# Performance work log

Hardware: AMD Instinct MI355X
Metric: run time of the kernel (lower is better)

Reference implementation:

```python
import jax, jax.numpy as jnp
import numpy as np

B, L, D, H = 2, 4096, 512, 8
DK = D // H
SCALE = 1.0 / float(np.sqrt(DK))


def setup_inputs() -> dict:
    key = jax.random.key(0)
    k1, k2, k3 = jax.random.split(key, 3)
    x = jax.random.normal(k1, (B, L, D), dtype=jnp.float32)
    w_qkv = jax.random.normal(k2, (3 * D, D), dtype=jnp.float32) * 0.02
    w_o = jax.random.normal(k3, (D, D), dtype=jnp.float32) * 0.02
    return {"x": x, "w_qkv": w_qkv, "w_o": w_o}


def reference(x, w_qkv, w_o):
    b, l, d = x.shape
    # qkv projection: Linear(d, 3d, bias=False) -> x @ W^T
    qkv = (x @ w_qkv.T).reshape(b, l, 3, H, DK).transpose(2, 0, 3, 1, 4)  # [3,B,H,L,dk]
    q, k, v = qkv[0], qkv[1], qkv[2]
    # naive O(L^2) attention (faithful to source)
    scores = jnp.einsum("bhld,bhmd->bhlm", q, k) * SCALE  # [B,H,L,L]
    attn = jax.nn.softmax(scores, axis=-1)
    ctx = jnp.einsum("bhlm,bhmd->bhld", attn, v)  # [B,H,L,dk]
    ctx = ctx.transpose(0, 2, 1, 3).reshape(b, l, d)
    return ctx @ w_o.T
```

## Files before the change

### kernel.cpp

```cpp
#include <hip/hip_runtime.h>


#define Bq 2
#define Lq 4096
#define Dq 512
#define Hq 8
#define DKq 64
#define PST 72

using short8  = __attribute__((ext_vector_type(8))) short;
using ushort8 = __attribute__((ext_vector_type(8))) unsigned short;
using float4v = __attribute__((ext_vector_type(4))) float;
using half4   = __attribute__((ext_vector_type(4))) _Float16;
typedef unsigned short u16;
typedef unsigned int   u32;

__device__ __forceinline__ u16 f2bf(float f) {
    u32 u = __float_as_uint(f);
    u += 0x7fffu + ((u >> 16) & 1u);
    return (u16)(u >> 16);
}

__device__ __forceinline__ float exp2fast(float x) {
#if __has_builtin(__builtin_amdgcn_exp2f)
    return __builtin_amdgcn_exp2f(x);
#else
    return exp2f(x);
#endif
}

__device__ __forceinline__ float4v mfma16(short8 a, short8 b, float4v c) {
    return __builtin_amdgcn_mfma_f32_16x16x32_bf16(a, b, c, 0, 0, 0);
}

__device__ __forceinline__ void gload_lds16(const u16* g, u16* l) {
    __builtin_amdgcn_global_load_lds(
        (const __attribute__((address_space(1))) unsigned int*)g,
        (__attribute__((address_space(3))) unsigned int*)l,
        16, 0, 0);
}

__global__ __launch_bounds__(256) void castall(const float* __restrict__ x,
                                               const float* __restrict__ wq,
                                               const float* __restrict__ wo,
                                               u16* __restrict__ xb,
                                               u16* __restrict__ wqb,
                                               u16* __restrict__ wob) {
    int g = blockIdx.x;
    const float* s; u16* d; int base;
    if (g < 4096)      { s = x;  d = xb;  base = g * 1024; }
    else if (g < 4864) { s = wq; d = wqb; base = (g - 4096) * 1024; }
    else               { s = wo; d = wob; base = (g - 4864) * 1024; }
    int i = base + threadIdx.x * 4;
    float4 f = *(const float4*)&s[i];
    ushort4 o;
    o.x = f2bf(f.x); o.y = f2bf(f.y); o.z = f2bf(f.z); o.w = f2bf(f.w);
    *(ushort4*)&d[i] = o;
}

__global__ __launch_bounds__(256) void qkv_gemm(const u16* __restrict__ A,
                                                const u16* __restrict__ Bw,
                                                u16* __restrict__ qb,
                                                u16* __restrict__ kb,
                                                u16* __restrict__ vt) {
    __shared__ __align__(16) union {
        struct { u16 A[128 * 64]; u16 B[128 * 64]; } s;
        u16 epi[128 * 134];
    } sm;
    const int m0 = blockIdx.x * 128, n0 = blockIdx.y * 128;
    const int tid = threadIdx.x, w = tid >> 6, lane = tid & 63;
    const int l15 = lane & 15, quad = lane >> 4;
    const int wy = w & 1, wx = w >> 1;
    const int r8 = lane >> 3, c8 = lane & 7, csw = c8 ^ r8;
    const int sw = l15 & 7;

    float4v acc[4][4];
    float4v zero = {0.f, 0.f, 0.f, 0.f};
#pragma unroll
    for (int mi = 0; mi < 4; mi++)
#pragma unroll
        for (int ni = 0; ni < 4; ni++) acc[mi][ni] = zero;

    for (int k0 = 0; k0 < 512; k0 += 64) {
#pragma unroll
        for (int i = 0; i < 4; i++) {
            int row = w * 32 + i * 8;
            gload_lds16(&A[(size_t)(m0 + row + r8) * 512 + k0 + csw * 8], &sm.s.A[row * 64]);
            gload_lds16(&Bw[(size_t)(n0 + row + r8) * 512 + k0 + csw * 8], &sm.s.B[row * 64]);
        }
        __syncthreads();
        short8 af0[4], af1[4], bf0[4], bf1[4];
#pragma unroll
        for (int t = 0; t < 4; t++) {
            int rowA = wy * 64 + t * 16 + l15;
            af0[t] = *(const short8*)&sm.s.A[rowA * 64 + ((quad ^ sw) * 8)];
            af1[t] = *(const short8*)&sm.s.A[rowA * 64 + (((quad + 4) ^ sw) * 8)];
            int rowB = wx * 64 + t * 16 + l15;
            bf0[t] = *(const short8*)&sm.s.B[rowB * 64 + ((quad ^ sw) * 8)];
            bf1[t] = *(const short8*)&sm.s.B[rowB * 64 + (((quad + 4) ^ sw) * 8)];
        }
#pragma unroll
        for (int mi = 0; mi < 4; mi++)
#pragma unroll
            for (int ni = 0; ni < 4; ni++) {
                acc[mi][ni] = mfma16(af0[mi], bf0[ni], acc[mi][ni]);
                acc[mi][ni] = mfma16(af1[mi], bf1[ni], acc[mi][ni]);
            }
        __syncthreads();
    }

    const int sel = n0 >> 9;
    if (sel < 2) {
        const float sc = (sel == 0) ? 0.18033688f : 1.0f;
#pragma unroll
        for (int mi = 0; mi < 4; mi++)
#pragma unroll
            for (int ni = 0; ni < 4; ni++)
#pragma unroll
                for (int r = 0; r < 4; r++)
                    sm.epi[(wy * 64 + mi * 16 + quad * 4 + r) * 134 + wx * 64 + ni * 16 + l15] =
                        f2bf(acc[mi][ni][r] * sc);
        __syncthreads();
        u16* tgt = (sel == 0) ? qb : kb;
#pragma unroll
        for (int i = 0; i < 8; i++) {
            int flat = i * 2048 + tid * 8;
            int row = flat >> 7, col = flat & 127;
            ushort8 vv = *(const ushort8*)&sm.epi[row * 134 + col];
            int dg = (n0 & 511) + col, h = dg >> 6, dk = dg & 63;
            int mm = m0 + row, b = mm >> 12, l = mm & 4095;
            *(ushort8*)&tgt[((size_t)(b * Hq + h) * Lq + l) * DKq + dk] = vv;
        }
    } else {
#pragma unroll
        for (int mi = 0; mi < 4; mi++)
#pragma unroll
            for (int ni = 0; ni < 4; ni++) {
                ushort4 v4;
                v4.x = f2bf(acc[mi][ni][0]); v4.y = f2bf(acc[mi][ni][1]);
                v4.z = f2bf(acc[mi][ni][2]); v4.w = f2bf(acc[mi][ni][3]);
                *(ushort4*)&sm.epi[(wx * 64 + ni * 16 + l15) * 134 + wy * 64 + mi * 16 + quad * 4] = v4;
            }
        __syncthreads();
#pragma unroll
        for (int i = 0; i < 8; i++) {
            int flat = i * 2048 + tid * 8;
            int vrow = flat >> 7, vcol = flat & 127;
            ushort8 vv = *(const ushort8*)&sm.epi[vrow * 134 + vcol];
            int dg = (n0 & 511) + vrow, h = dg >> 6, dk = dg & 63;
            int mm = m0 + vcol, b = mm >> 12, l = mm & 4095;
            *(ushort8*)&vt[((size_t)(b * Hq + h) * DKq + dk) * Lq + l] = vv;
        }
    }
}

__global__ __launch_bounds__(256, 4) void attn_kern(const u16* __restrict__ qb,
                                                    const u16* __restrict__ kb,
                                                    const u16* __restrict__ vt,
                                                    _Float16* __restrict__ op0,
                                                    _Float16* __restrict__ op1,
                                                    float* __restrict__ denp) {
    __shared__ __align__(16) u16 Ks[64 * 64];
    __shared__ __align__(16) u16 Vs[64 * 64];
    __shared__ __align__(16) u16 Ps[4 * 32 * PST];
    const int g = blockIdx.x;
    const int xcd = g & 7, idx = g >> 3;
    const int bh = xcd * 2 + (idx & 1);
    const int rest = idx >> 1;
    const int split = rest & 1;
    const int q0 = (rest >> 1) * 128;
    const int tid = threadIdx.x;
    const int w = tid >> 6, lane = tid & 63, l15 = lane & 15, quad = lane >> 4;
    const int r8 = lane >> 3, c8 = lane & 7, csw = c8 ^ r8;
    const int sw = l15 & 7;

    const u16* qbase = qb + (size_t)bh * Lq * DKq;
    const u16* kbase = kb + (size_t)bh * Lq * DKq;
    const u16* vbase = vt + (size_t)bh * DKq * Lq;

    short8 aq0[2], aq1[2];
#pragma unroll
    for (int s = 0; s < 2; s++) {
        int qrow = q0 + w * 32 + s * 16 + l15;
        aq0[s] = *(const short8*)&qbase[(size_t)qrow * DKq + quad * 8];
        aq1[s] = *(const short8*)&qbase[(size_t)qrow * DKq + 32 + quad * 8];
    }

    short8 ones8;
#pragma unroll
    for (int j = 0; j < 8; j++) ones8[j] = (short)0x3F80;

    float4v zero = {0.f, 0.f, 0.f, 0.f};
    float4v oacc[2][4], den[2];
#pragma unroll
    for (int s = 0; s < 2; s++) {
        den[s] = zero;
#pragma unroll
        for (int n = 0; n < 4; n++) oacc[s][n] = zero;
    }

    u16* Pw = Ps + w * 32 * PST;
    const int j0base = split * 2048;

    for (int jt = 0; jt < 32; jt++) {
        int j0 = j0base + jt * 64;
        if (w < 2) {
#pragma unroll
            for (int i = 0; i < 4; i++) {
                int base = w * 32 + i * 8;
                gload_lds16(&kbase[(size_t)(j0 + base + r8) * DKq + csw * 8], &Ks[base * 64]);
            }
        } else {
#pragma unroll
            for (int i = 0; i < 4; i++) {
                int base = (w - 2) * 32 + i * 8;
                gload_lds16(&vbase[(size_t)(base + r8) * Lq + j0 + csw * 8], &Vs[base * 64]);
            }
        }
        __syncthreads();

        short8 kf0[4], kf1[4], vf0[4], vf1[4];
#pragma unroll
        for (int n = 0; n < 4; n++) {
            int row = n * 16 + l15;
            kf0[n] = *(const short8*)&Ks[row * 64 + ((quad ^ sw) * 8)];
            kf1[n] = *(const short8*)&Ks[row * 64 + (((quad + 4) ^ sw) * 8)];
            vf0[n] = *(const short8*)&Vs[row * 64 + ((quad ^ sw) * 8)];
            vf1[n] = *(const short8*)&Vs[row * 64 + (((quad + 4) ^ sw) * 8)];
        }

#pragma unroll
        for (int s = 0; s < 2; s++) {
#pragma unroll
            for (int nk = 0; nk < 4; nk++) {
                float4v sv = zero;
                sv = mfma16(kf0[nk], aq0[s], sv);
                sv = mfma16(kf1[nk], aq1[s], sv);
                u32 u0 = __float_as_uint(exp2fast(sv[0])) + 0x8000u;
                u32 u1 = __float_as_uint(exp2fast(sv[1])) + 0x8000u;
                u32 u2 = __float_as_uint(exp2fast(sv[2])) + 0x8000u;
                u32 u3 = __float_as_uint(exp2fast(sv[3])) + 0x8000u;
                uint2 pv;
                pv.x = __builtin_amdgcn_perm(u1, u0, 0x07060302u);
                pv.y = __builtin_amdgcn_perm(u3, u2, 0x07060302u);
                *(uint2*)&Pw[(s * 16 + l15) * PST + nk * 16 + quad * 4] = pv;
            }
        }

#pragma unroll
        for (int s = 0; s < 2; s++) {
            short8 ap0 = *(const short8*)&Pw[(s * 16 + l15) * PST + quad * 8];
            short8 ap1 = *(const short8*)&Pw[(s * 16 + l15) * PST + 32 + quad * 8];
            den[s] = mfma16(ap0, ones8, den[s]);
            den[s] = mfma16(ap1, ones8, den[s]);
#pragma unroll
            for (int n = 0; n < 4; n++) {
                oacc[s][n] = mfma16(ap0, vf0[n], oacc[s][n]);
                oacc[s][n] = mfma16(ap1, vf1[n], oacc[s][n]);
            }
        }
        __syncthreads();
    }

    _Float16* op = split ? op1 : op0;
#pragma unroll
    for (int s = 0; s < 2; s++)
#pragma unroll
        for (int r = 0; r < 4; r++) {
            float dv = den[s][r];
            float rd = __builtin_amdgcn_rcpf(dv);
            int row = q0 + w * 32 + s * 16 + quad * 4 + r;
            if (l15 == 0) denp[(size_t)(split * 16 + bh) * Lq + row] = dv;
#pragma unroll
            for (int n = 0; n < 4; n++)
                op[((size_t)bh * Lq + row) * DKq + n * 16 + l15] =
                    (_Float16)(oacc[s][n][r] * rd);
        }
}

__global__ __launch_bounds__(256) void combine(const _Float16* __restrict__ op0,
                                               const _Float16* __restrict__ op1,
                                               const float* __restrict__ denp,
                                               u16* __restrict__ ctxq) {
    int t = blockIdx.x * 256 + threadIdx.x;
    int dk4 = t & 15, l = (t >> 4) & 4095, bh = t >> 16;
    size_t r0 = (size_t)bh * Lq + l;
    half4 h0 = *(const half4*)&op0[r0 * DKq + dk4 * 4];
    half4 h1 = *(const half4*)&op1[r0 * DKq + dk4 * 4];
    float d0 = denp[r0];
    float d1 = denp[(size_t)(16 + bh) * Lq + l];
    float rs = __builtin_amdgcn_rcpf(d0 + d1);
    int b = bh >> 3, h = bh & 7;
    ushort4 o;
    o.x = f2bf(((float)h0.x * d0 + (float)h1.x * d1) * rs);
    o.y = f2bf(((float)h0.y * d0 + (float)h1.y * d1) * rs);
    o.z = f2bf(((float)h0.z * d0 + (float)h1.z * d1) * rs);
    o.w = f2bf(((float)h0.w * d0 + (float)h1.w * d1) * rs);
    *(ushort4*)&ctxq[((size_t)(b * Lq + l)) * Dq + h * DKq + dk4 * 4] = o;
}

__global__ __launch_bounds__(256) void out_gemm(const u16* __restrict__ A,
                                                const u16* __restrict__ Bw,
                                                float* __restrict__ out) {
    __shared__ __align__(16) union {
        struct { u16 A[128 * 64]; u16 B[128 * 64]; } s;
        float fepi[64 * 132];
    } sm;
    const int m0 = blockIdx.x * 128, n0 = blockIdx.y * 128;
    const int tid = threadIdx.x, w = tid >> 6, lane = tid & 63;
    const int l15 = lane & 15, quad = lane >> 4;
    const int wy = w & 1, wx = w >> 1;
    const int r8 = lane >> 3, c8 = lane & 7, csw = c8 ^ r8;
    const int sw = l15 & 7;

    float4v acc[4][4];
    float4v zero = {0.f, 0.f, 0.f, 0.f};
#pragma unroll
    for (int mi = 0; mi < 4; mi++)
#pragma unroll
        for (int ni = 0; ni < 4; ni++) acc[mi][ni] = zero;

    for (int k0 = 0; k0 < 512; k0 += 64) {
#pragma unroll
        for (int i = 0; i < 4; i++) {
            int row = w * 32 + i * 8;
            gload_lds16(&A[(size_t)(m0 + row + r8) * 512 + k0 + csw * 8], &sm.s.A[row * 64]);
            gload_lds16(&Bw[(size_t)(n0 + row + r8) * 512 + k0 + csw * 8], &sm.s.B[row * 64]);
        }
        __syncthreads();
        short8 af0[4], af1[4], bf0[4], bf1[4];
#pragma unroll
        for (int t = 0; t < 4; t++) {
            int rowA = wy * 64 + t * 16 + l15;
            af0[t] = *(const short8*)&sm.s.A[rowA * 64 + ((quad ^ sw) * 8)];
            af1[t] = *(const short8*)&sm.s.A[rowA * 64 + (((quad + 4) ^ sw) * 8)];
            int rowB = wx * 64 + t * 16 + l15;
            bf0[t] = *(const short8*)&sm.s.B[rowB * 64 + ((quad ^ sw) * 8)];
            bf1[t] = *(const short8*)&sm.s.B[rowB * 64 + (((quad + 4) ^ sw) * 8)];
        }
#pragma unroll
        for (int mi = 0; mi < 4; mi++)
#pragma unroll
            for (int ni = 0; ni < 4; ni++) {
                acc[mi][ni] = mfma16(af0[mi], bf0[ni], acc[mi][ni]);
                acc[mi][ni] = mfma16(af1[mi], bf1[ni], acc[mi][ni]);
            }
        __syncthreads();
    }

#pragma unroll
    for (int ph = 0; ph < 2; ph++) {
#pragma unroll
        for (int mh = 0; mh < 2; mh++) {
            int mi = ph * 2 + mh;
            int lr = wy * 32 + mh * 16 + quad * 4;
#pragma unroll
            for (int ni = 0; ni < 4; ni++)
#pragma unroll
                for (int r = 0; r < 4; r++)
                    sm.fepi[(lr + r) * 132 + wx * 64 + ni * 16 + l15] = acc[mi][ni][r];
        }
        __syncthreads();
#pragma unroll
        for (int i = 0; i < 8; i++) {
            int flat = i * 1024 + tid * 4;
            int lrow = flat >> 7, col = flat & 127;
            float4 vv = *(const float4*)&sm.fepi[lrow * 132 + col];
            int m = (lrow & 31) + (lrow >> 5) * 64 + ph * 32;
            *(float4*)&out[(size_t)(m0 + m) * 512 + n0 + col] = vv;
        }
        __syncthreads();
    }
}

extern "C" void kernel_launch(void* const* d_in, const int* in_sizes, int n_in,
                              void* d_out, int out_size, void* d_ws, size_t ws_size,
                              hipStream_t stream) {
    const float* x     = (const float*)d_in[0];
    const float* w_qkv = (const float*)d_in[1];
    const float* w_o   = (const float*)d_in[2];
    float* out = (float*)d_out;

    const size_t N_X   = (size_t)Bq * Lq * Dq;
    const size_t N_WQ  = (size_t)3 * Dq * Dq;
    const size_t N_WO  = (size_t)Dq * Dq;
    const size_t N_QKV = (size_t)Bq * Hq * Lq * DKq;

    u16* xb  = (u16*)d_ws;
    u16* wqb = xb + N_X;
    u16* wob = wqb + N_WQ;
    u16* qb  = wob + N_WO;
    u16* kb  = qb + N_QKV;
    u16* vt  = kb + N_QKV;
    u16* o1r = vt + N_QKV;

    _Float16* op0  = (_Float16*)xb;
    _Float16* op1  = (_Float16*)o1r;
    float*    denp = (float*)wqb;
    u16*      ctxq = qb;

    castall<<<dim3(5120), 256, 0, stream>>>(x, w_qkv, w_o, xb, wqb, wob);
    qkv_gemm<<<dim3(64, 12), 256, 0, stream>>>(xb, wqb, qb, kb, vt);
    attn_kern<<<dim3(1024), 256, 0, stream>>>(qb, kb, vt, op0, op1, denp);
    combine<<<dim3(4096), 256, 0, stream>>>(op0, op1, denp, ctxq);
    out_gemm<<<dim3(64, 4), 256, 0, stream>>>(ctxq, wob, out);
}
```

Before: 197.1 us.

## Double-buffer K/V tiles and feed P straight from registers into 16x16x16 MFMA

The attention loop now double-buffers the K/V tiles in LDS, prefetching the next tile before computing the current one, which leaves one barrier per iteration instead of two. The P tile no longer makes a round trip through shared memory: each exp'd score fragment is packed in registers and fed directly to 16x16x16 bf16 MFMAs, with V read in a matching 4-element layout. Launch bounds drop to 3 waves per EU to allow more registers, and a dummy pad write adjusts LDS size. This trades more MFMA instructions of smaller K and lower occupancy for less LDS traffic and fewer barriers.

Result: no change. 200.2 us (+1.6%).

```diff
diff --git a/kernel.cpp b/kernel.cpp
--- a/kernel.cpp
+++ b/kernel.cpp
@@ -6,9 +6,9 @@
 #define Dq 512
 #define Hq 8
 #define DKq 64
-#define PST 72
 
 using short8  = __attribute__((ext_vector_type(8))) short;
+using short4v = __attribute__((ext_vector_type(4))) short;
 using ushort8 = __attribute__((ext_vector_type(8))) unsigned short;
 using float4v = __attribute__((ext_vector_type(4))) float;
 using half4   = __attribute__((ext_vector_type(4))) _Float16;
@@ -31,6 +31,17 @@
 
 __device__ __forceinline__ float4v mfma16(short8 a, short8 b, float4v c) {
     return __builtin_amdgcn_mfma_f32_16x16x32_bf16(a, b, c, 0, 0, 0);
+}
+
+__device__ __forceinline__ float4v mfma1k(short4v a, short4v b, float4v c) {
+#if __has_builtin(__builtin_amdgcn_mfma_f32_16x16x16bf16_1k)
+    return __builtin_amdgcn_mfma_f32_16x16x16bf16_1k(a, b, c, 0, 0, 0);
+#else
+    float4v d;
+    asm volatile("v_mfma_f32_16x16x16_bf16 %0, %1, %2, %3"
+                 : "=v"(d) : "v"(a), "v"(b), "v"(c));
+    return d;
+#endif
 }
 
 __device__ __forceinline__ void gload_lds16(const u16* g, u16* l) {
@@ -154,15 +165,14 @@
     }
 }
 
-__global__ __launch_bounds__(256, 4) void attn_kern(const u16* __restrict__ qb,
+__global__ __launch_bounds__(256, 3) void attn_kern(const u16* __restrict__ qb,
                                                     const u16* __restrict__ kb,
                                                     const u16* __restrict__ vt,
                                                     _Float16* __restrict__ op0,
                                                     _Float16* __restrict__ op1,
                                                     float* __restrict__ denp) {
-    __shared__ __align__(16) u16 Ks[64 * 64];
-    __shared__ __align__(16) u16 Vs[64 * 64];
-    __shared__ __align__(16) u16 Ps[4 * 32 * PST];
+    __shared__ __align__(16) u16 KV[2][2][64 * 64];
+    __shared__ __align__(16) u16 pad[256];
     const int g = blockIdx.x;
     const int xcd = g & 7, idx = g >> 3;
     const int bh = xcd * 2 + (idx & 1);
@@ -174,6 +184,8 @@
     const int r8 = lane >> 3, c8 = lane & 7, csw = c8 ^ r8;
     const int sw = l15 & 7;
 
+    if (denp == (float*)1) pad[tid & 255] = (u16)tid;
+
     const u16* qbase = qb + (size_t)bh * Lq * DKq;
     const u16* kbase = kb + (size_t)bh * Lq * DKq;
     const u16* vbase = vt + (size_t)bh * DKq * Lq;
@@ -186,10 +198,7 @@
         aq1[s] = *(const short8*)&qbase[(size_t)qrow * DKq + 32 + quad * 8];
     }
 
-    short8 ones8;
-#pragma unroll
-    for (int j = 0; j < 8; j++) ones8[j] = (short)0x3F80;
-
+    short4v ones4 = {(short)0x3F80, (short)0x3F80, (short)0x3F80, (short)0x3F80};
     float4v zero = {0.f, 0.f, 0.f, 0.f};
     float4v oacc[2][4], den[2];
 #pragma unroll
@@ -199,67 +208,75 @@
         for (int n = 0; n < 4; n++) oacc[s][n] = zero;
     }
 
-    u16* Pw = Ps + w * 32 * PST;
     const int j0base = split * 2048;
 
-    for (int jt = 0; jt < 32; jt++) {
-        int j0 = j0base + jt * 64;
+    {
         if (w < 2) {
 #pragma unroll
             for (int i = 0; i < 4; i++) {
                 int base = w * 32 + i * 8;
-                gload_lds16(&kbase[(size_t)(j0 + base + r8) * DKq + csw * 8], &Ks[base * 64]);
+                gload_lds16(&kbase[(size_t)(j0base + base + r8) * DKq + csw * 8], &KV[0][0][base * 64]);
             }
         } else {
 #pragma unroll
             for (int i = 0; i < 4; i++) {
                 int base = (w - 2) * 32 + i * 8;
-                gload_lds16(&vbase[(size_t)(base + r8) * Lq + j0 + csw * 8], &Vs[base * 64]);
-            }
-        }
-        __syncthreads();
-
-        short8 kf0[4], kf1[4], vf0[4], vf1[4];
-#pragma unroll
-        for (int n = 0; n < 4; n++) {
-            int row = n * 16 + l15;
-            kf0[n] = *(const short8*)&Ks[row * 64 + ((quad ^ sw) * 8)];
-            kf1[n] = *(const short8*)&Ks[row * 64 + (((quad + 4) ^ sw) * 8)];
-            vf0[n] = *(const short8*)&Vs[row * 64 + ((quad ^ sw) * 8)];
-            vf1[n] = *(const short8*)&Vs[row * 64 + (((quad + 4) ^ sw) * 8)];
-        }
-
-#pragma unroll
-        for (int s = 0; s < 2; s++) {
-#pragma unroll
-            for (int nk = 0; nk < 4; nk++) {
-                float4v sv = zero;
-                sv = mfma16(kf0[nk], aq0[s], sv);
-                sv = mfma16(kf1[nk], aq1[s], sv);
+                gload_lds16(&vbase[(size_t)(base + r8) * Lq + j0base + csw * 8], &KV[0][1][base * 64]);
+            }
+        }
+    }
+
+    int p = 0;
+    for (int jt = 0; jt < 32; jt++) {
+        __syncthreads();
+        if (jt < 31) {
+            int j0 = j0base + (jt + 1) * 64;
+            if (w < 2) {
+#pragma unroll
+                for (int i = 0; i < 4; i++) {
+                    int base = w * 32 + i * 8;
+                    gload_lds16(&kbase[(size_t)(j0 + base + r8) * DKq + csw * 8], &KV[p ^ 1][0][base * 64]);
+                }
+            } else {
+#pragma unroll
+                for (int i = 0; i < 4; i++) {
+                    int base = (w - 2) * 32 + i * 8;
+                    gload_lds16(&vbase[(size_t)(base + r8) * Lq + j0 + csw * 8], &KV[p ^ 1][1][base * 64]);
+                }
+            }
+        }
+        const u16* Kb = KV[p][0];
+        const u16* Vb = KV[p][1];
+
+#pragma unroll
+        for (int nk = 0; nk < 4; nk++) {
+            int krow = nk * 16 + l15;
+            short8 k0 = *(const short8*)&Kb[krow * 64 + ((quad ^ sw) * 8)];
+            short8 k1 = *(const short8*)&Kb[krow * 64 + (((quad + 4) ^ sw) * 8)];
+            int voff = ((nk * 2 + (quad >> 1)) ^ sw) * 8 + (quad & 1) * 4;
+            short4v vk[4];
+#pragma unroll
+            for (int n = 0; n < 4; n++)
+                vk[n] = *(const short4v*)&Vb[(n * 16 + l15) * 64 + voff];
+#pragma unroll
+            for (int s = 0; s < 2; s++) {
+                float4v sv = mfma16(k0, aq0[s], zero);
+                sv = mfma16(k1, aq1[s], sv);
                 u32 u0 = __float_as_uint(exp2fast(sv[0])) + 0x8000u;
                 u32 u1 = __float_as_uint(exp2fast(sv[1])) + 0x8000u;
                 u32 u2 = __float_as_uint(exp2fast(sv[2])) + 0x8000u;
                 u32 u3 = __float_as_uint(exp2fast(sv[3])) + 0x8000u;
-                uint2 pv;
-                pv.x = __builtin_amdgcn_perm(u1, u0, 0x07060302u);
-                pv.y = __builtin_amdgcn_perm(u3, u2, 0x07060302u);
-                *(uint2*)&Pw[(s * 16 + l15) * PST + nk * 16 + quad * 4] = pv;
-            }
-        }
-
-#pragma unroll
-        for (int s = 0; s < 2; s++) {
-            short8 ap0 = *(const short8*)&Pw[(s * 16 + l15) * PST + quad * 8];
-            short8 ap1 = *(const short8*)&Pw[(s * 16 + l15) * PST + 32 + quad * 8];
-            den[s] = mfma16(ap0, ones8, den[s]);
-            den[s] = mfma16(ap1, ones8, den[s]);
-#pragma unroll
-            for (int n = 0; n < 4; n++) {
-                oacc[s][n] = mfma16(ap0, vf0[n], oacc[s][n]);
-                oacc[s][n] = mfma16(ap1, vf1[n], oacc[s][n]);
-            }
-        }
-        __syncthreads();
+                union { uint2 u; short4v s4; } cv;
+                cv.u.x = __builtin_amdgcn_perm(u1, u0, 0x07060302u);
+                cv.u.y = __builtin_amdgcn_perm(u3, u2, 0x07060302u);
+                short4v pf = cv.s4;
+                den[s] = mfma1k(pf, ones4, den[s]);
+#pragma unroll
+                for (int n = 0; n < 4; n++)
+                    oacc[s][n] = mfma1k(pf, vk[n], oacc[s][n]);
+            }
+        }
+        p ^= 1;
     }
 
     _Float16* op = split ? op1 : op0;
```

## Fuse split-attention combine into output projection GEMM A-tile load

Applied to the files above, without the earlier changes.

Removes the separate combine kernel. The output GEMM now reads both fp16 partial attention outputs and their denominators, merges and normalizes them, and writes bf16 directly into the shared-memory A tile, so the intermediate ctx buffer is never written or read back. The N tile shrinks from 128 to 64, doubling the grid to 64x8 blocks to make up for the heavier A load. The cost is that each block repeats the combine arithmetic for the A rows it shares with other N-tiles, and the A load becomes synchronous register loads instead of async global-to-LDS copies.

Measured after the change: 203.0 us. 3.0% more time.

```diff
diff --git a/kernel.cpp b/kernel.cpp
--- a/kernel.cpp
+++ b/kernel.cpp
@@ -11,7 +11,6 @@
 using short8  = __attribute__((ext_vector_type(8))) short;
 using ushort8 = __attribute__((ext_vector_type(8))) unsigned short;
 using float4v = __attribute__((ext_vector_type(4))) float;
-using half4   = __attribute__((ext_vector_type(4))) _Float16;
 typedef unsigned short u16;
 typedef unsigned int   u32;
 
@@ -278,70 +277,73 @@
         }
 }
 
-__global__ __launch_bounds__(256) void combine(const _Float16* __restrict__ op0,
-                                               const _Float16* __restrict__ op1,
-                                               const float* __restrict__ denp,
-                                               u16* __restrict__ ctxq) {
-    int t = blockIdx.x * 256 + threadIdx.x;
-    int dk4 = t & 15, l = (t >> 4) & 4095, bh = t >> 16;
-    size_t r0 = (size_t)bh * Lq + l;
-    half4 h0 = *(const half4*)&op0[r0 * DKq + dk4 * 4];
-    half4 h1 = *(const half4*)&op1[r0 * DKq + dk4 * 4];
-    float d0 = denp[r0];
-    float d1 = denp[(size_t)(16 + bh) * Lq + l];
-    float rs = __builtin_amdgcn_rcpf(d0 + d1);
-    int b = bh >> 3, h = bh & 7;
-    ushort4 o;
-    o.x = f2bf(((float)h0.x * d0 + (float)h1.x * d1) * rs);
-    o.y = f2bf(((float)h0.y * d0 + (float)h1.y * d1) * rs);
-    o.z = f2bf(((float)h0.z * d0 + (float)h1.z * d1) * rs);
-    o.w = f2bf(((float)h0.w * d0 + (float)h1.w * d1) * rs);
-    *(ushort4*)&ctxq[((size_t)(b * Lq + l)) * Dq + h * DKq + dk4 * 4] = o;
-}
-
-__global__ __launch_bounds__(256) void out_gemm(const u16* __restrict__ A,
+__global__ __launch_bounds__(256) void out_gemm(const _Float16* __restrict__ op0,
+                                                const _Float16* __restrict__ op1,
+                                                const float* __restrict__ denp,
                                                 const u16* __restrict__ Bw,
                                                 float* __restrict__ out) {
     __shared__ __align__(16) union {
-        struct { u16 A[128 * 64]; u16 B[128 * 64]; } s;
-        float fepi[64 * 132];
+        struct { u16 A[128 * 64]; u16 B[64 * 64]; } s;
+        float fepi[64 * 68];
     } sm;
-    const int m0 = blockIdx.x * 128, n0 = blockIdx.y * 128;
+    const int m0 = blockIdx.x * 128, n0 = blockIdx.y * 64;
     const int tid = threadIdx.x, w = tid >> 6, lane = tid & 63;
     const int l15 = lane & 15, quad = lane >> 4;
-    const int wy = w & 1, wx = w >> 1;
+    const int wy = w & 1, wx = (w >> 1) & 1;
     const int r8 = lane >> 3, c8 = lane & 7, csw = c8 ^ r8;
     const int sw = l15 & 7;
 
-    float4v acc[4][4];
+    float4v acc[4][2];
     float4v zero = {0.f, 0.f, 0.f, 0.f};
 #pragma unroll
     for (int mi = 0; mi < 4; mi++)
 #pragma unroll
-        for (int ni = 0; ni < 4; ni++) acc[mi][ni] = zero;
+        for (int ni = 0; ni < 2; ni++) acc[mi][ni] = zero;
 
     for (int k0 = 0; k0 < 512; k0 += 64) {
+        const int kk = k0 >> 6;
+#pragma unroll
+        for (int i = 0; i < 2; i++) {
+            int row = w * 16 + i * 8;
+            gload_lds16(&Bw[(size_t)(n0 + row + r8) * 512 + k0 + csw * 8], &sm.s.B[row * 64]);
+        }
 #pragma unroll
         for (int i = 0; i < 4; i++) {
             int row = w * 32 + i * 8;
-            gload_lds16(&A[(size_t)(m0 + row + r8) * 512 + k0 + csw * 8], &sm.s.A[row * 64]);
-            gload_lds16(&Bw[(size_t)(n0 + row + r8) * 512 + k0 + csw * 8], &sm.s.B[row * 64]);
-        }
-        __syncthreads();
-        short8 af0[4], af1[4], bf0[4], bf1[4];
+            int mm = m0 + row + r8;
+            int b = mm >> 12, l = mm & 4095;
+            int bh = b * Hq + kk;
+            size_t rowoff = ((size_t)bh * Lq + l) * DKq + csw * 8;
+            union { float4 f; _Float16 h[8]; } ua, ub;
+            ua.f = *(const float4*)&op0[rowoff];
+            ub.f = *(const float4*)&op1[rowoff];
+            float d0 = denp[(size_t)bh * Lq + l];
+            float d1 = denp[(size_t)(16 + bh) * Lq + l];
+            float rs = __builtin_amdgcn_rcpf(d0 + d1);
+            ushort8 ov;
+#pragma unroll
+            for (int j = 0; j < 8; j++)
+                ov[j] = f2bf(((float)ua.h[j] * d0 + (float)ub.h[j] * d1) * rs);
+            *(ushort8*)&sm.s.A[(row + r8) * 64 + c8 * 8] = ov;
+        }
+        __syncthreads();
+        short8 af0[4], af1[4], bf0[2], bf1[2];
 #pragma unroll
         for (int t = 0; t < 4; t++) {
             int rowA = wy * 64 + t * 16 + l15;
             af0[t] = *(const short8*)&sm.s.A[rowA * 64 + ((quad ^ sw) * 8)];
             af1[t] = *(const short8*)&sm.s.A[rowA * 64 + (((quad + 4) ^ sw) * 8)];
-            int rowB = wx * 64 + t * 16 + l15;
+        }
+#pragma unroll
+        for (int t = 0; t < 2; t++) {
+            int rowB = wx * 32 + t * 16 + l15;
             bf0[t] = *(const short8*)&sm.s.B[rowB * 64 + ((quad ^ sw) * 8)];
             bf1[t] = *(const short8*)&sm.s.B[rowB * 64 + (((quad + 4) ^ sw) * 8)];
         }
 #pragma unroll
         for (int mi = 0; mi < 4; mi++)
 #pragma unroll
-            for (int ni = 0; ni < 4; ni++) {
+            for (int ni = 0; ni < 2; ni++) {
                 acc[mi][ni] = mfma16(af0[mi], bf0[ni], acc[mi][ni]);
                 acc[mi][ni] = mfma16(af1[mi], bf1[ni], acc[mi][ni]);
             }
@@ -355,17 +357,17 @@
             int mi = ph * 2 + mh;
             int lr = wy * 32 + mh * 16 + quad * 4;
 #pragma unroll
-            for (int ni = 0; ni < 4; ni++)
+            for (int ni = 0; ni < 2; ni++)
 #pragma unroll
                 for (int r = 0; r < 4; r++)
-                    sm.fepi[(lr + r) * 132 + wx * 64 + ni * 16 + l15] = acc[mi][ni][r];
-        }
-        __syncthreads();
-#pragma unroll
-        for (int i = 0; i < 8; i++) {
+                    sm.fepi[(lr + r) * 68 + wx * 32 + ni * 16 + l15] = acc[mi][ni][r];
+        }
+        __syncthreads();
+#pragma unroll
+        for (int i = 0; i < 4; i++) {
             int flat = i * 1024 + tid * 4;
-            int lrow = flat >> 7, col = flat & 127;
-            float4 vv = *(const float4*)&sm.fepi[lrow * 132 + col];
+            int lrow = flat >> 6, col = flat & 63;
+            float4 vv = *(const float4*)&sm.fepi[lrow * 68 + col];
             int m = (lrow & 31) + (lrow >> 5) * 64 + ph * 32;
             *(float4*)&out[(size_t)(m0 + m) * 512 + n0 + col] = vv;
         }
@@ -397,11 +399,9 @@
     _Float16* op0  = (_Float16*)xb;
     _Float16* op1  = (_Float16*)o1r;
     float*    denp = (float*)wqb;
-    u16*      ctxq = qb;
 
     castall<<<dim3(5120), 256, 0, stream>>>(x, w_qkv, w_o, xb, wqb, wob);
     qkv_gemm<<<dim3(64, 12), 256, 0, stream>>>(xb, wqb, qb, kb, vt);
     attn_kern<<<dim3(1024), 256, 0, stream>>>(qb, kb, vt, op0, op1, denp);
-    combine<<<dim3(4096), 256, 0, stream>>>(op0, op1, denp, ctxq);
-    out_gemm<<<dim3(64, 4), 256, 0, stream>>>(ctxq, wob, out);
-}
+    out_gemm<<<dim3(64, 8), 256, 0, stream>>>(op0, op1, denp, wob, out);
+}
```
